# Kernel tuning notes

Measured on AMD Instinct MI355X. Metric: run time of the kernel, lower is better.

Reference implementation:

```python
import jax, jax.numpy as jnp
import numpy as np

N_CLASSES = 9
INPUT_SIZE = N_CLASSES + 1  # 10
HIDDEN = 512
BATCH = 256
SEQ = 1024


def setup_inputs() -> dict:
    key = jax.random.key(0)
    ks = jax.random.split(key, 7)
    s_ih = 1.0 / np.sqrt(HIDDEN)
    inputs = jax.random.normal(ks[0], (BATCH, SEQ, INPUT_SIZE), dtype=jnp.float32)
    # LSTMCell params (PyTorch layout: [4H, in], gate order i,f,g,o)
    W_ih = jax.random.uniform(ks[1], (4 * HIDDEN, INPUT_SIZE), jnp.float32, -s_ih, s_ih)
    W_hh = jax.random.uniform(ks[2], (4 * HIDDEN, HIDDEN), jnp.float32, -s_ih, s_ih)
    b_ih = jax.random.uniform(ks[3], (4 * HIDDEN,), jnp.float32, -s_ih, s_ih)
    b_hh = jax.random.uniform(ks[4], (4 * HIDDEN,), jnp.float32, -s_ih, s_ih)
    # Output projection: kaiming_normal_ (fan_in = HIDDEN, relu gain sqrt(2)), zero bias
    lin_W = jax.random.normal(ks[5], (N_CLASSES, HIDDEN), dtype=jnp.float32) * np.float32(np.sqrt(2.0 / HIDDEN))
    lin_b = jnp.zeros((N_CLASSES,), dtype=jnp.float32)
    return {"inputs": inputs, "W_ih": W_ih, "W_hh": W_hh, "b_ih": b_ih,
            "b_hh": b_hh, "lin_W": lin_W, "lin_b": lin_b}


def reference(inputs, W_ih, W_hh, b_ih, b_hh, lin_W, lin_b):
    B = inputs.shape[0]
    H = W_hh.shape[1]
    # Precompute input contributions for all steps in one big GEMM: [B,T,4H]
    x_gates = jnp.einsum('bti,gi->btg', inputs, W_ih) + b_ih + b_hh

    def step(carry, xg_t):
        h, c = carry
        gates = xg_t + h @ W_hh.T  # [B, 4H]
        i, f, g, o = jnp.split(gates, 4, axis=-1)
        i = jax.nn.sigmoid(i)
        f = jax.nn.sigmoid(f)
        g = jnp.tanh(g)
        o = jax.nn.sigmoid(o)
        c = f * c + i * g
        h = o * jnp.tanh(c)
        return (h, c), h

    h0 = jnp.zeros((B, H), dtype=inputs.dtype)
    c0 = jnp.zeros((B, H), dtype=inputs.dtype)
    _, hs = jax.lax.scan(step, (h0, c0), jnp.swapaxes(x_gates, 0, 1))  # hs: [T,B,H]
    # Per-step Linear, batched into one GEMM: [B,T,n_classes]
    logits = jnp.einsum('tbh,ch->btc', hs, lin_W) + lin_b
    return logits
```

## Files before the change

kernel.cpp:

```cpp
#include <hip/hip_runtime.h>

typedef unsigned int u32;
typedef unsigned long long u64;
typedef unsigned short u16;
typedef short bfrag __attribute__((ext_vector_type(8)));
typedef float f4 __attribute__((ext_vector_type(4)));
typedef u32 u32x4 __attribute__((ext_vector_type(4)));

#define HID 512
#define SEQT 1024
#define NIN 10
#define NC 9
#define NCL 16
#define MB  16
#define KSN 17
#define COLS 544
#define XC0 512
#define ONECOL 522
#define LROW 552

#define WPACK_U16 (16*4*2*KSN*64*8)
#define WPACK_BYTES (WPACK_U16*2)
#define HEX_U16 (NCL*2*MB*COLS)
#define HEX_BYTES (HEX_U16*2)
#define FLAGS_U32 (NCL*64)
#define FLAGS_BYTES (FLAGS_U32*4)

__device__ __forceinline__ u16 f2b(float f){
  u32 u = __float_as_uint(f);
  return (u16)((u + 0x7fffu + ((u>>16)&1u)) >> 16);
}
__device__ __forceinline__ float b2f(u16 b){ return __uint_as_float(((u32)b)<<16); }
__device__ __forceinline__ float sigm(float x){ return 1.f/(1.f+__expf(-x)); }
__device__ __forceinline__ float tanh_(float x){ float e=__expf(2.f*x); return 1.f - 2.f/(e+1.f); }

__device__ __forceinline__ u32 ldflag(u64 base, u32 off){
  u32 r;
  asm volatile("global_load_dword %0, %1, %2 sc0 sc1\n\ts_waitcnt vmcnt(0)"
               : "=&v"(r) : "v"(off), "s"(base) : "memory");
  return r;
}
__device__ __forceinline__ void st32_sys(u64 base, u32 off, u32 v){
  asm volatile("global_store_dword %0, %1, %2 sc0 sc1"
               :: "v"(off), "v"(v), "s"(base) : "memory");
}
__device__ __forceinline__ void st16_sys(u64 base, u32 off, u16 v){
  asm volatile("global_store_short %0, %1, %2 sc0 sc1"
               :: "v"(off), "v"((u32)v), "s"(base) : "memory");
}
__device__ __forceinline__ void drain_vm(){
  asm volatile("s_waitcnt vmcnt(0)" ::: "memory");
}
__device__ __forceinline__ void spin_flags(u64 flgb, u32 foff, u32 tgt){
  int guard = 0;
  for(;;){
    u32 v = ldflag(flgb, foff);
    if (__all((int)(v >= tgt))) break;
    if (++guard > 50000) break;
  }
}

__global__ void pack_kernel(const float* __restrict__ W_ih, const float* __restrict__ W_hh,
                            const float* __restrict__ b_ih, const float* __restrict__ b_hh,
                            u16* __restrict__ Wpack)
{
  int tid = blockIdx.x*256 + threadIdx.x;
  if (tid >= 16*4*2*KSN*64) return;
  int lane = tid & 63;
  int rest = tid >> 6;
  int ks = rest % KSN; rest /= KSN;
  int p = rest & 1; rest >>= 1;
  int w = rest & 3; rest >>= 2;
  int g = rest;
  int c2 = lane & 15;
  int kb = lane >> 4;
  int j = g*32 + w*8 + (c2 & 7);
  int gate = (p ? 2 : 0) + (c2 >= 8 ? 1 : 0);
  int R = gate*HID + j;

  union { u16 s[8]; bfrag v; } o;
  if (ks < 16) {
    const float* src = W_hh + (size_t)R*HID + ks*32 + kb*8;
    #pragma unroll
    for (int e=0;e<8;e++) o.s[e] = f2b(src[e]);
  } else {
    #pragma unroll
    for (int e=0;e<8;e++) {
      int k = kb*8 + e;
      float v = (k < NIN) ? W_ih[(size_t)R*NIN + k] : (k==NIN ? (b_ih[R]+b_hh[R]) : 0.f);
      o.s[e] = f2b(v);
    }
  }
  *(bfrag*)(Wpack + (size_t)tid*8) = o.v;
}

__global__ void init_kernel(const float* __restrict__ inputs, u16* __restrict__ hex_,
                            u32* __restrict__ flags)
{
  int tid = blockIdx.x*256 + threadIdx.x;
  if (tid < HEX_U16) {
    int col = tid % COLS;
    int rest = tid / COLS;
    int row = rest % MB; rest /= MB;
    int buf = rest & 1;
    int c = rest >> 1;
    u16 v = 0;
    if (col >= XC0) {
      if (col == ONECOL) v = f2b(1.0f);
      else if (col < ONECOL) {
        if (buf == 0) v = f2b(inputs[((size_t)(c*MB+row)*SEQT + 0)*NIN + (col-XC0)]);
      }
    }
    hex_[tid] = v;
  }
  if (tid < FLAGS_U32) flags[tid] = 0;
}

__global__ __launch_bounds__(256, 1) void lstm_kernel(
    const float* __restrict__ inputs, const float* __restrict__ lin_W,
    const float* __restrict__ lin_b, const u16* __restrict__ Wpack,
    u16* __restrict__ hex_, u32* __restrict__ flags, float* __restrict__ out)
{
  const int bid = blockIdx.x;
  const int cl = bid >> 4;
  const int g = bid & 15;
  const int tid = threadIdx.x;
  const int w = tid >> 6;
  const int lane = tid & 63;
  const int c2 = lane & 15;
  const int kb = lane >> 4;
  const int jb = g*32 + w*8;
  const bool lowhalf = (c2 < 8);
  const int vb = cl*MB + g;

  __shared__ __align__(16) u16 panel[MB*LROW];

  bfrag wf0[KSN], wf1[KSN];
  {
    const u16* base = Wpack + ((size_t)(g*4+w)*2)*KSN*64*8;
    #pragma unroll
    for (int ks=0;ks<KSN;ks++) wf0[ks] = *(const bfrag*)(base + ((size_t)ks*64 + lane)*8);
    #pragma unroll
    for (int ks=0;ks<KSN;ks++) wf1[ks] = *(const bfrag*)(base + ((size_t)(KSN+ks)*64 + lane)*8);
  }
  float lw[3][8]; float lb[3];
  if (w < 3) {
    #pragma unroll
    for (int cc=0;cc<3;cc++){
      int cls = w*3+cc;
      lb[cc] = lin_b[cls];
      #pragma unroll
      for (int e=0;e<8;e++) lw[cc][e] = lin_W[(size_t)cls*HID + lane*8 + e];
    }
  }

  float cst[4] = {0.f,0.f,0.f,0.f};

  const u64 ex0 = (u64)(hex_ + (size_t)(cl*2+0)*MB*COLS);
  const u64 ex1 = (u64)(hex_ + (size_t)(cl*2+1)*MB*COLS);
  const u64 flgb = (u64)(flags + (size_t)cl*64);
  const u32 foff = (u32)(c2*4);

  u32 goff[4], loff[4], goff4, loff4;
  #pragma unroll
  for (int i=0;i<4;i++){
    u32 chunk = (u32)tid + (u32)i*256u;
    u32 row = chunk / 68u, rem = chunk - row*68u;
    goff[i] = row*1088u + rem*16u;
    loff[i] = row*(LROW*2u) + rem*16u;
  }
  {
    u32 chunk = 1024u + (u32)lane;
    u32 row = chunk / 68u, rem = chunk - row*68u;
    goff4 = row*1088u + rem*16u;
    loff4 = row*(LROW*2u) + rem*16u;
  }

  for (int t = 0; t < SEQT; ++t) {
    const u64 cur = (t & 1) ? ex1 : ex0;
    const u64 nxt = (t & 1) ? ex0 : ex1;

    spin_flags(flgb, foff, (u32)t);

    {
      u32x4 r0,r1,r2,r3;
      if (w == 3) {
        u32x4 r4;
        asm volatile(
          "global_load_dwordx4 %0, %5, %10 sc0 sc1\n\t"
          "global_load_dwordx4 %1, %6, %10 sc0 sc1\n\t"
          "global_load_dwordx4 %2, %7, %10 sc0 sc1\n\t"
          "global_load_dwordx4 %3, %8, %10 sc0 sc1\n\t"
          "global_load_dwordx4 %4, %9, %10 sc0 sc1\n\t"
          "s_waitcnt vmcnt(0)"
          : "=&v"(r0), "=&v"(r1), "=&v"(r2), "=&v"(r3), "=&v"(r4)
          : "v"(goff[0]), "v"(goff[1]), "v"(goff[2]), "v"(goff[3]), "v"(goff4), "s"(cur)
          : "memory");
        *(u32x4*)((char*)panel + loff[0]) = r0;
        *(u32x4*)((char*)panel + loff[1]) = r1;
        *(u32x4*)((char*)panel + loff[2]) = r2;
        *(u32x4*)((char*)panel + loff[3]) = r3;
        *(u32x4*)((char*)panel + loff4)   = r4;
      } else {
        asm volatile(
          "global_load_dwordx4 %0, %4, %8 sc0 sc1\n\t"
          "global_load_dwordx4 %1, %5, %8 sc0 sc1\n\t"
          "global_load_dwordx4 %2, %6, %8 sc0 sc1\n\t"
          "global_load_dwordx4 %3, %7, %8 sc0 sc1\n\t"
          "s_waitcnt vmcnt(0)"
          : "=&v"(r0), "=&v"(r1), "=&v"(r2), "=&v"(r3)
          : "v"(goff[0]), "v"(goff[1]), "v"(goff[2]), "v"(goff[3]), "s"(cur)
          : "memory");
        *(u32x4*)((char*)panel + loff[0]) = r0;
        *(u32x4*)((char*)panel + loff[1]) = r1;
        *(u32x4*)((char*)panel + loff[2]) = r2;
        *(u32x4*)((char*)panel + loff[3]) = r3;
      }
    }
    __syncthreads();

    float xv = 0.f;
    if (w==0 && lane < NIN && t+1 < SEQT)
      xv = inputs[((size_t)vb*SEQT + (t+1))*NIN + lane];

    bfrag hx;
    if (w < 3) hx = *(const bfrag*)&panel[g*LROW + lane*8];

    f4 acc0 = {0.f,0.f,0.f,0.f}, acc1 = {0.f,0.f,0.f,0.f};
    #pragma unroll
    for (int ks=0;ks<KSN;ks++){
      bfrag av = *(const bfrag*)&panel[c2*LROW + ks*32 + kb*8];
      acc0 = __builtin_amdgcn_mfma_f32_16x16x32_bf16(av, wf0[ks], acc0, 0,0,0);
      acc1 = __builtin_amdgcn_mfma_f32_16x16x32_bf16(av, wf1[ks], acc1, 0,0,0);
    }

    u16 hb[4];
    #pragma unroll
    for (int r=0;r<4;r++){
      float a0 = sigm(acc0[r]);
      float a1 = lowhalf ? tanh_(acc1[r]) : sigm(acc1[r]);
      float p0 = __shfl_xor(a0, 8, 64);
      float p1 = __shfl_xor(a1, 8, 64);
      float ii = lowhalf ? a0 : p0;
      float ff = lowhalf ? p0 : a0;
      float gg = lowhalf ? a1 : p1;
      float oo = lowhalf ? p1 : a1;
      float cn = ff*cst[r] + ii*gg;
      cst[r] = cn;
      hb[r] = f2b(oo * tanh_(cn));
    }

    #pragma unroll
    for (int r=0;r<4;r++){
      u32 nb = (u32)(u16)__shfl_down((int)hb[r], 1, 64);
      if (lowhalf && !(c2 & 1)) {
        u32 pv = (u32)hb[r] | (nb << 16);
        st32_sys(nxt, (u32)(((kb*4+r)*COLS + jb + c2)*2), pv);
      }
    }
    if (w==0 && lane < NIN && t+1 < SEQT)
      st16_sys(nxt, (u32)((g*COLS + XC0 + lane)*2), f2b(xv));

    drain_vm();
    __syncthreads();
    if (tid == 0)
      st32_sys(flgb, (u32)(g*4), (u32)(t+1));

    if (w < 3 && t > 0) {
      float hv[8];
      #pragma unroll
      for (int e=0;e<8;e++) hv[e] = b2f((u16)hx[e]);
      #pragma unroll
      for (int cc=0;cc<3;cc++){
        float s = 0.f;
        #pragma unroll
        for (int e=0;e<8;e++) s += hv[e]*lw[cc][e];
        #pragma unroll
        for (int off=1;off<64;off<<=1) s += __shfl_xor(s, off, 64);
        if (lane == 0)
          out[((size_t)vb*SEQT + (t-1))*NC + (w*3+cc)] = s + lb[cc];
      }
    }
  }

  spin_flags(flgb, foff, (u32)SEQT);
  if (w < 3) {
    u32x4 rr;
    asm volatile("global_load_dwordx4 %0, %1, %2 sc0 sc1\n\ts_waitcnt vmcnt(0)"
                 : "=&v"(rr) : "v"((u32)((g*COLS + lane*8)*2)), "s"(ex0) : "memory");
    float hv[8];
    #pragma unroll
    for (int e=0;e<4;e++){
      hv[2*e]   = b2f((u16)(rr[e] & 0xffffu));
      hv[2*e+1] = b2f((u16)(rr[e] >> 16));
    }
    #pragma unroll
    for (int cc=0;cc<3;cc++){
      float s = 0.f;
      #pragma unroll
      for (int e=0;e<8;e++) s += hv[e]*lw[cc][e];
      #pragma unroll
      for (int off=1;off<64;off<<=1) s += __shfl_xor(s, off, 64);
      if (lane == 0)
        out[((size_t)vb*SEQT + (SEQT-1))*NC + (w*3+cc)] = s + lb[cc];
    }
  }
}

extern "C" void kernel_launch(void* const* d_in, const int* in_sizes, int n_in,
                              void* d_out, int out_size, void* d_ws, size_t ws_size,
                              hipStream_t stream)
{
  const float* inputs = (const float*)d_in[0];
  const float* W_ih   = (const float*)d_in[1];
  const float* W_hh   = (const float*)d_in[2];
  const float* b_ih   = (const float*)d_in[3];
  const float* b_hh   = (const float*)d_in[4];
  const float* lin_W  = (const float*)d_in[5];
  const float* lin_b  = (const float*)d_in[6];

  u16* Wpack = (u16*)d_ws;
  u16* hex_  = (u16*)((char*)d_ws + WPACK_BYTES);
  u32* flags = (u32*)((char*)d_ws + WPACK_BYTES + HEX_BYTES);

  pack_kernel<<<(16*4*2*KSN*64 + 255)/256, 256, 0, stream>>>(W_ih, W_hh, b_ih, b_hh, Wpack);
  init_kernel<<<(HEX_U16 + 255)/256, 256, 0, stream>>>(inputs, hex_, flags);
  lstm_kernel<<<256, 256, 0, stream>>>(inputs, lin_W, lin_b, Wpack, hex_, flags, (float*)d_out);
}
```

Baseline: 3.481 ms.

## Decouple x-input from exchange buffer, per-wave flags, wider h stores, deferred projection

Each lane now loads the x inputs directly and feeds them as a separate final MFMA fragment, so the global h-exchange rows hold only the 512 hidden values and no longer carry x or bias columns. The block-wide barrier before the flag store is removed: each wave publishes its own flag and wave 0 polls all 64 flags with two loads in flight. h is packed into 128-bit stores, and the output projection is delayed one step and placed in the shadow of the exchange loads. This shortens the per-step critical path of the recurrent loop and costs more flag traffic plus a more involved pipeline.

```diff
diff --git a/kernel.cpp b/kernel.cpp
--- a/kernel.cpp
+++ b/kernel.cpp
@@ -14,14 +14,12 @@
 #define NCL 16
 #define MB  16
 #define KSN 17
-#define COLS 544
-#define XC0 512
-#define ONECOL 522
-#define LROW 552
+#define HROW 512
+#define LROW 516
 
 #define WPACK_U16 (16*4*2*KSN*64*8)
 #define WPACK_BYTES (WPACK_U16*2)
-#define HEX_U16 (NCL*2*MB*COLS)
+#define HEX_U16 (NCL*2*MB*HROW)
 #define HEX_BYTES (HEX_U16*2)
 #define FLAGS_U32 (NCL*64)
 #define FLAGS_BYTES (FLAGS_U32*4)
@@ -34,30 +32,30 @@
 __device__ __forceinline__ float sigm(float x){ return 1.f/(1.f+__expf(-x)); }
 __device__ __forceinline__ float tanh_(float x){ float e=__expf(2.f*x); return 1.f - 2.f/(e+1.f); }
 
-__device__ __forceinline__ u32 ldflag(u64 base, u32 off){
-  u32 r;
-  asm volatile("global_load_dword %0, %1, %2 sc0 sc1\n\ts_waitcnt vmcnt(0)"
-               : "=&v"(r) : "v"(off), "s"(base) : "memory");
-  return r;
-}
 __device__ __forceinline__ void st32_sys(u64 base, u32 off, u32 v){
-  asm volatile("global_store_dword %0, %1, %2 sc0 sc1"
-               :: "v"(off), "v"(v), "s"(base) : "memory");
-}
-__device__ __forceinline__ void st16_sys(u64 base, u32 off, u16 v){
-  asm volatile("global_store_short %0, %1, %2 sc0 sc1"
-               :: "v"(off), "v"((u32)v), "s"(base) : "memory");
+  asm volatile("global_store_dword %0, %1, %2 sc0 sc1" :: "v"(off), "v"(v), "s"(base) : "memory");
+}
+__device__ __forceinline__ void st128_sys(u64 base, u32 off, u32x4 v){
+  asm volatile("global_store_dwordx4 %0, %1, %2 sc0 sc1" :: "v"(off), "v"(v), "s"(base) : "memory");
 }
 __device__ __forceinline__ void drain_vm(){
   asm volatile("s_waitcnt vmcnt(0)" ::: "memory");
 }
 __device__ __forceinline__ void spin_flags(u64 flgb, u32 foff, u32 tgt){
+  u32 v0, v1 = 0;
+  asm volatile("global_load_dword %0, %1, %2 sc0 sc1" : "=&v"(v0) : "v"(foff), "s"(flgb) : "memory");
   int guard = 0;
   for(;;){
-    u32 v = ldflag(flgb, foff);
-    if (__all((int)(v >= tgt))) break;
-    if (++guard > 50000) break;
-  }
+    asm volatile("global_load_dword %0, %1, %2 sc0 sc1\n\ts_waitcnt vmcnt(1)"
+                 : "=&v"(v1) : "v"(foff), "s"(flgb) : "memory");
+    if (__all((int)(v0 >= tgt))) break;
+    asm volatile("global_load_dword %0, %1, %2 sc0 sc1\n\ts_waitcnt vmcnt(1)"
+                 : "=&v"(v0) : "v"(foff), "s"(flgb) : "memory");
+    if (__all((int)(v1 >= tgt))) break;
+    if ((guard += 2) > 400000) break;
+  }
+  drain_vm();
+  asm volatile("" :: "v"(v0), "v"(v1));
 }
 
 __global__ void pack_kernel(const float* __restrict__ W_ih, const float* __restrict__ W_hh,
@@ -94,25 +92,10 @@
   *(bfrag*)(Wpack + (size_t)tid*8) = o.v;
 }
 
-__global__ void init_kernel(const float* __restrict__ inputs, u16* __restrict__ hex_,
-                            u32* __restrict__ flags)
+__global__ void init_kernel(u16* __restrict__ hex_, u32* __restrict__ flags)
 {
   int tid = blockIdx.x*256 + threadIdx.x;
-  if (tid < HEX_U16) {
-    int col = tid % COLS;
-    int rest = tid / COLS;
-    int row = rest % MB; rest /= MB;
-    int buf = rest & 1;
-    int c = rest >> 1;
-    u16 v = 0;
-    if (col >= XC0) {
-      if (col == ONECOL) v = f2b(1.0f);
-      else if (col < ONECOL) {
-        if (buf == 0) v = f2b(inputs[((size_t)(c*MB+row)*SEQT + 0)*NIN + (col-XC0)]);
-      }
-    }
-    hex_[tid] = v;
-  }
+  if (tid < HEX_U16) hex_[tid] = 0;
   if (tid < FLAGS_U32) flags[tid] = 0;
 }
 
@@ -134,6 +117,7 @@
   const int vb = cl*MB + g;
 
   __shared__ __align__(16) u16 panel[MB*LROW];
+  __shared__ __align__(16) u16 rowbuf[2][HID];
 
   bfrag wf0[KSN], wf1[KSN];
   {
@@ -156,83 +140,88 @@
 
   float cst[4] = {0.f,0.f,0.f,0.f};
 
-  const u64 ex0 = (u64)(hex_ + (size_t)(cl*2+0)*MB*COLS);
-  const u64 ex1 = (u64)(hex_ + (size_t)(cl*2+1)*MB*COLS);
+  const u64 ex0 = (u64)(hex_ + (size_t)(cl*2+0)*MB*HROW);
+  const u64 ex1 = (u64)(hex_ + (size_t)(cl*2+1)*MB*HROW);
   const u64 flgb = (u64)(flags + (size_t)cl*64);
-  const u32 foff = (u32)(c2*4);
-
-  u32 goff[4], loff[4], goff4, loff4;
+  const u32 foff = (u32)(lane*4);
+
+  u32 go[4], lo[4];
   #pragma unroll
   for (int i=0;i<4;i++){
     u32 chunk = (u32)tid + (u32)i*256u;
-    u32 row = chunk / 68u, rem = chunk - row*68u;
-    goff[i] = row*1088u + rem*16u;
-    loff[i] = row*(LROW*2u) + rem*16u;
-  }
-  {
-    u32 chunk = 1024u + (u32)lane;
-    u32 row = chunk / 68u, rem = chunk - row*68u;
-    goff4 = row*1088u + rem*16u;
-    loff4 = row*(LROW*2u) + rem*16u;
-  }
+    go[i] = (chunk>>6)*1024u + (chunk&63u)*16u;
+    lo[i] = (chunk>>6)*(LROW*2u) + (chunk&63u)*16u;
+  }
+
+  const float* xrow = inputs + (size_t)(cl*MB + c2)*SEQT*NIN;
 
   for (int t = 0; t < SEQT; ++t) {
     const u64 cur = (t & 1) ? ex1 : ex0;
     const u64 nxt = (t & 1) ? ex0 : ex1;
 
-    spin_flags(flgb, foff, (u32)t);
-
+    union { u32 u[4]; bfrag v; } xu;
+    xu.u[0]=0; xu.u[1]=0; xu.u[2]=0; xu.u[3]=0;
     {
-      u32x4 r0,r1,r2,r3;
-      if (w == 3) {
-        u32x4 r4;
-        asm volatile(
-          "global_load_dwordx4 %0, %5, %10 sc0 sc1\n\t"
-          "global_load_dwordx4 %1, %6, %10 sc0 sc1\n\t"
-          "global_load_dwordx4 %2, %7, %10 sc0 sc1\n\t"
-          "global_load_dwordx4 %3, %8, %10 sc0 sc1\n\t"
-          "global_load_dwordx4 %4, %9, %10 sc0 sc1\n\t"
-          "s_waitcnt vmcnt(0)"
-          : "=&v"(r0), "=&v"(r1), "=&v"(r2), "=&v"(r3), "=&v"(r4)
-          : "v"(goff[0]), "v"(goff[1]), "v"(goff[2]), "v"(goff[3]), "v"(goff4), "s"(cur)
-          : "memory");
-        *(u32x4*)((char*)panel + loff[0]) = r0;
-        *(u32x4*)((char*)panel + loff[1]) = r1;
-        *(u32x4*)((char*)panel + loff[2]) = r2;
-        *(u32x4*)((char*)panel + loff[3]) = r3;
-        *(u32x4*)((char*)panel + loff4)   = r4;
-      } else {
-        asm volatile(
-          "global_load_dwordx4 %0, %4, %8 sc0 sc1\n\t"
-          "global_load_dwordx4 %1, %5, %8 sc0 sc1\n\t"
-          "global_load_dwordx4 %2, %6, %8 sc0 sc1\n\t"
-          "global_load_dwordx4 %3, %7, %8 sc0 sc1\n\t"
-          "s_waitcnt vmcnt(0)"
-          : "=&v"(r0), "=&v"(r1), "=&v"(r2), "=&v"(r3)
-          : "v"(goff[0]), "v"(goff[1]), "v"(goff[2]), "v"(goff[3]), "s"(cur)
-          : "memory");
-        *(u32x4*)((char*)panel + loff[0]) = r0;
-        *(u32x4*)((char*)panel + loff[1]) = r1;
-        *(u32x4*)((char*)panel + loff[2]) = r2;
-        *(u32x4*)((char*)panel + loff[3]) = r3;
-      }
-    }
+      const float* p = xrow + (size_t)t*NIN;
+      if (kb == 0) {
+        #pragma unroll
+        for (int q=0;q<4;q++) xu.u[q] = (u32)f2b(p[2*q]) | ((u32)f2b(p[2*q+1])<<16);
+      } else if (kb == 1) {
+        xu.u[0] = (u32)f2b(p[8]) | ((u32)f2b(p[9])<<16);
+        xu.u[1] = 0x3F80u;
+      }
+    }
+
+    if (w == 0) spin_flags(flgb, foff, (u32)t);
     __syncthreads();
 
-    float xv = 0.f;
-    if (w==0 && lane < NIN && t+1 < SEQT)
-      xv = inputs[((size_t)vb*SEQT + (t+1))*NIN + lane];
-
-    bfrag hx;
-    if (w < 3) hx = *(const bfrag*)&panel[g*LROW + lane*8];
+    u32x4 r0,r1,r2,r3;
+    asm volatile(
+      "global_load_dwordx4 %0, %4, %8 sc0 sc1\n\t"
+      "global_load_dwordx4 %1, %5, %8 sc0 sc1\n\t"
+      "global_load_dwordx4 %2, %6, %8 sc0 sc1\n\t"
+      "global_load_dwordx4 %3, %7, %8 sc0 sc1"
+      : "=&v"(r0), "=&v"(r1), "=&v"(r2), "=&v"(r3)
+      : "v"(go[0]), "v"(go[1]), "v"(go[2]), "v"(go[3]), "s"(cur)
+      : "memory");
+
+    if (w < 3 && t >= 2) {
+      bfrag hx = *(const bfrag*)&rowbuf[(t-1)&1][lane*8];
+      float hv[8];
+      #pragma unroll
+      for (int e=0;e<8;e++) hv[e] = b2f((u16)hx[e]);
+      #pragma unroll
+      for (int cc=0;cc<3;cc++){
+        float s = 0.f;
+        #pragma unroll
+        for (int e=0;e<8;e++) s += hv[e]*lw[cc][e];
+        #pragma unroll
+        for (int off=1;off<64;off<<=1) s += __shfl_xor(s, off, 64);
+        if (lane == 0)
+          out[((size_t)vb*SEQT + (t-2))*NC + (w*3+cc)] = s + lb[cc];
+      }
+    }
+
+    drain_vm();
+    __builtin_amdgcn_sched_barrier(0);
+    *(u32x4*)((char*)panel + lo[0]) = r0;
+    *(u32x4*)((char*)panel + lo[1]) = r1;
+    *(u32x4*)((char*)panel + lo[2]) = r2;
+    *(u32x4*)((char*)panel + lo[3]) = r3;
+    __syncthreads();
+
+    if (w == 3)
+      *(bfrag*)&rowbuf[t&1][lane*8] = *(const bfrag*)&panel[g*LROW + lane*8];
 
     f4 acc0 = {0.f,0.f,0.f,0.f}, acc1 = {0.f,0.f,0.f,0.f};
     #pragma unroll
-    for (int ks=0;ks<KSN;ks++){
+    for (int ks=0;ks<16;ks++){
       bfrag av = *(const bfrag*)&panel[c2*LROW + ks*32 + kb*8];
       acc0 = __builtin_amdgcn_mfma_f32_16x16x32_bf16(av, wf0[ks], acc0, 0,0,0);
       acc1 = __builtin_amdgcn_mfma_f32_16x16x32_bf16(av, wf1[ks], acc1, 0,0,0);
     }
+    acc0 = __builtin_amdgcn_mfma_f32_16x16x32_bf16(xu.v, wf0[16], acc0, 0,0,0);
+    acc1 = __builtin_amdgcn_mfma_f32_16x16x32_bf16(xu.v, wf1[16], acc1, 0,0,0);
 
     u16 hb[4];
     #pragma unroll
@@ -252,21 +241,26 @@
 
     #pragma unroll
     for (int r=0;r<4;r++){
-      u32 nb = (u32)(u16)__shfl_down((int)hb[r], 1, 64);
-      if (lowhalf && !(c2 & 1)) {
-        u32 pv = (u32)hb[r] | (nb << 16);
-        st32_sys(nxt, (u32)(((kb*4+r)*COLS + jb + c2)*2), pv);
-      }
-    }
-    if (w==0 && lane < NIN && t+1 < SEQT)
-      st16_sys(nxt, (u32)((g*COLS + XC0 + lane)*2), f2b(xv));
+      u32 pv = (u32)hb[r] | (((u32)(u16)__shfl_down((int)hb[r], 1, 64)) << 16);
+      u32 p1 = __shfl_down(pv, 2, 64);
+      u32 p2 = __shfl_down(pv, 4, 64);
+      u32 p3 = __shfl_down(pv, 6, 64);
+      if (c2 == 0) {
+        u32x4 pk = {pv, p1, p2, p3};
+        st128_sys(nxt, (u32)((kb*4+r)*1024 + jb*2), pk);
+      }
+    }
 
     drain_vm();
-    __syncthreads();
-    if (tid == 0)
-      st32_sys(flgb, (u32)(g*4), (u32)(t+1));
-
-    if (w < 3 && t > 0) {
+    if (lane == 0)
+      st32_sys(flgb, (u32)((g*4+w)*4), (u32)(t+1));
+  }
+
+  if (w == 0) spin_flags(flgb, foff, (u32)SEQT);
+  __syncthreads();
+  if (w < 3) {
+    {
+      bfrag hx = *(const bfrag*)&rowbuf[(SEQT-1)&1][lane*8];
       float hv[8];
       #pragma unroll
       for (int e=0;e<8;e++) hv[e] = b2f((u16)hx[e]);
@@ -278,31 +272,29 @@
         #pragma unroll
         for (int off=1;off<64;off<<=1) s += __shfl_xor(s, off, 64);
         if (lane == 0)
-          out[((size_t)vb*SEQT + (t-1))*NC + (w*3+cc)] = s + lb[cc];
-      }
-    }
-  }
-
-  spin_flags(flgb, foff, (u32)SEQT);
-  if (w < 3) {
-    u32x4 rr;
-    asm volatile("global_load_dwordx4 %0, %1, %2 sc0 sc1\n\ts_waitcnt vmcnt(0)"
-                 : "=&v"(rr) : "v"((u32)((g*COLS + lane*8)*2)), "s"(ex0) : "memory");
-    float hv[8];
-    #pragma unroll
-    for (int e=0;e<4;e++){
-      hv[2*e]   = b2f((u16)(rr[e] & 0xffffu));
-      hv[2*e+1] = b2f((u16)(rr[e] >> 16));
-    }
-    #pragma unroll
-    for (int cc=0;cc<3;cc++){
-      float s = 0.f;
-      #pragma unroll
-      for (int e=0;e<8;e++) s += hv[e]*lw[cc][e];
-      #pragma unroll
-      for (int off=1;off<64;off<<=1) s += __shfl_xor(s, off, 64);
-      if (lane == 0)
-        out[((size_t)vb*SEQT + (SEQT-1))*NC + (w*3+cc)] = s + lb[cc];
+          out[((size_t)vb*SEQT + (SEQT-2))*NC + (w*3+cc)] = s + lb[cc];
+      }
+    }
+    {
+      u32x4 rr;
+      asm volatile("global_load_dwordx4 %0, %1, %2 sc0 sc1\n\ts_waitcnt vmcnt(0)"
+                   : "=&v"(rr) : "v"((u32)(g*1024 + lane*16)), "s"(ex0) : "memory");
+      float hv[8];
+      #pragma unroll
+      for (int e=0;e<4;e++){
+        hv[2*e]   = b2f((u16)(rr[e] & 0xffffu));
+        hv[2*e+1] = b2f((u16)(rr[e] >> 16));
+      }
+      #pragma unroll
+      for (int cc=0;cc<3;cc++){
+        float s = 0.f;
+        #pragma unroll
+        for (int e=0;e<8;e++) s += hv[e]*lw[cc][e];
+        #pragma unroll
+        for (int off=1;off<64;off<<=1) s += __shfl_xor(s, off, 64);
+        if (lane == 0)
+          out[((size_t)vb*SEQT + (SEQT-1))*NC + (w*3+cc)] = s + lb[cc];
+      }
     }
   }
 }
@@ -324,6 +316,6 @@
   u32* flags = (u32*)((char*)d_ws + WPACK_BYTES + HEX_BYTES);
 
   pack_kernel<<<(16*4*2*KSN*64 + 255)/256, 256, 0, stream>>>(W_ih, W_hh, b_ih, b_hh, Wpack);
-  init_kernel<<<(HEX_U16 + 255)/256, 256, 0, stream>>>(inputs, hex_, flags);
+  init_kernel<<<(HEX_U16 + 255)/256, 256, 0, stream>>>(hex_, flags);
   lstm_kernel<<<256, 256, 0, stream>>>(inputs, lin_W, lin_b, Wpack, hex_, flags, (float*)d_out);
 }
```

Measured after the change: 4.223 ms. 21.3% more time.
